# Kernel optimization log

Hardware: AMD Instinct MI355X
Metric: run time of the kernel (lower is better)

The kernel has to match this reference:

```python
import jax, jax.numpy as jnp
import numpy as np

B, L = 2, 256
CHAR, WORD = 8000, 50000
CE, WE, HID, REL = 128, 128, 256, 24
IN_DIM = CE + WE


def _lstm(x, mask, W, U, b):
    # Keras LSTM cell: z = x@W + h@U + b split into (i,f,g,o); masked steps carry state through.
    # x: (B, T, D) float, mask: (B, T) bool
    h0 = jnp.zeros((x.shape[0], U.shape[0]), x.dtype)

    def step(carry, xm):
        h, c = carry
        xt, mt = xm
        z = xt @ W + h @ U + b
        i, f, g, o = jnp.split(z, 4, axis=-1)
        c_new = jax.nn.sigmoid(f) * c + jax.nn.sigmoid(i) * jnp.tanh(g)
        h_new = jax.nn.sigmoid(o) * jnp.tanh(c_new)
        m = mt[:, None]
        h2 = jnp.where(m, h_new, h)
        c2 = jnp.where(m, c_new, c)
        return (h2, c2), h2

    _, hs = jax.lax.scan(step, (h0, h0), (jnp.swapaxes(x, 0, 1), jnp.swapaxes(mask, 0, 1)))
    return jnp.swapaxes(hs, 0, 1)  # (B, T, HID)


def _head(enc, Wu, bu, Wv, bv, Wuv, buv, Wc, bc):
    # Original: tile relu(u) over axis 1 (depends on j) and relu(v) over axis 2 (depends on i),
    # concat -> Dense. Equivalent fused form: split Wuv and broadcast-add the two projections.
    u = jax.nn.relu(enc @ Wu + bu)  # (B, L, E)
    v = jax.nn.relu(enc @ Wv + bv)  # (B, L, E)
    E = Wu.shape[1]
    uv = (jnp.einsum('bjd,de->bje', u, Wuv[:E])[:, None, :, :]
          + jnp.einsum('bid,de->bie', v, Wuv[E:])[:, :, None, :]
          + buv)  # (B, L, L, E)
    return uv @ Wc + bc  # (B, L, L, out)


def setup_inputs() -> dict:
    key = jax.random.key(0)
    ks = jax.random.split(key, 64)

    def w(k, shape):
        return jax.random.normal(k, shape, jnp.float32) * 0.05

    inp = {
        'inputs': jax.random.randint(ks[0], (B, L), 0, CHAR, jnp.int32),
        'input_words': jax.random.randint(ks[1], (B, L), 0, WORD, jnp.int32),
        'input_max_len': L,
        'embed_table': w(ks[2], (CHAR, CE)),
        'word_embed_table': w(ks[3], (WORD, WE)),
        'lstm_fwd_W': w(ks[4], (IN_DIM, 4 * HID)),
        'lstm_fwd_U': w(ks[5], (HID, 4 * HID)),
        'lstm_fwd_b': jnp.zeros((4 * HID,), jnp.float32),
        'lstm_bwd_W': w(ks[6], (IN_DIM, 4 * HID)),
        'lstm_bwd_U': w(ks[7], (HID, 4 * HID)),
        'lstm_bwd_b': jnp.zeros((4 * HID,), jnp.float32),
    }
    i = 8
    for name, out in (('eh', 1), ('hh', REL), ('tt', REL)):
        inp[f'{name}_u_W'] = w(ks[i], (2 * HID, CE)); i += 1
        inp[f'{name}_u_b'] = jnp.zeros((CE,), jnp.float32)
        inp[f'{name}_v_W'] = w(ks[i], (2 * HID, CE)); i += 1
        inp[f'{name}_v_b'] = jnp.zeros((CE,), jnp.float32)
        inp[f'{name}_uv_W'] = w(ks[i], (2 * CE, CE)); i += 1
        inp[f'{name}_uv_b'] = jnp.zeros((CE,), jnp.float32)
        inp[f'{name}_cls_W'] = w(ks[i], (CE, out)); i += 1
        inp[f'{name}_cls_b'] = jnp.zeros((out,), jnp.float32)
    return inp


def reference(inputs, input_words, input_max_len, embed_table, word_embed_table,
              lstm_fwd_W, lstm_fwd_U, lstm_fwd_b, lstm_bwd_W, lstm_bwd_U, lstm_bwd_b,
              eh_u_W, eh_u_b, eh_v_W, eh_v_b, eh_uv_W, eh_uv_b, eh_cls_W, eh_cls_b,
              hh_u_W, hh_u_b, hh_v_W, hh_v_b, hh_uv_W, hh_uv_b, hh_cls_W, hh_cls_b,
              tt_u_W, tt_u_b, tt_v_W, tt_v_b, tt_uv_W, tt_uv_b, tt_cls_W, tt_cls_b):
    mask = inputs != 0  # (B, L)
    x = jnp.concatenate([embed_table[inputs], word_embed_table[input_words]], axis=-1)
    h_fwd = _lstm(x, mask, lstm_fwd_W, lstm_fwd_U, lstm_fwd_b)
    h_bwd = _lstm(x[:, ::-1], mask[:, ::-1], lstm_bwd_W, lstm_bwd_U, lstm_bwd_b)[:, ::-1]
    enc = jnp.concatenate([h_fwd, h_bwd], axis=-1)  # (B, L, 2*HID)
    eh = jax.nn.sigmoid(_head(enc, eh_u_W, eh_u_b, eh_v_W, eh_v_b, eh_uv_W, eh_uv_b, eh_cls_W, eh_cls_b))
    hh = jax.nn.softmax(_head(enc, hh_u_W, hh_u_b, hh_v_W, hh_v_b, hh_uv_W, hh_uv_b, hh_cls_W, hh_cls_b), axis=-1)
    tt = jax.nn.softmax(_head(enc, tt_u_W, tt_u_b, tt_v_W, tt_v_b, tt_uv_W, tt_uv_b, tt_cls_W, tt_cls_b), axis=-1)
    return (eh, hh, tt)
```

## Files before the change

### kernel.cpp

```cpp
#include <hip/hip_runtime.h>
#include <hip/hip_bf16.h>

typedef unsigned short u16;
typedef unsigned int u32;

#define LSEQ 256

constexpr int XW_F  = 0;
constexpr int XW_B  = 524288;
constexpr int HF_O  = 1048576;
constexpr int HB_O  = 1179648;
constexpr int UV_O  = 1310720;
constexpr int PEH_O = 1703936;
constexpr int QEH_O = 1704448;
constexpr int PHH_O = 1704960;
constexpr int QHH_O = 1717248;
constexpr int PTT_O = 1729536;
constexpr int QTT_O = 1741824;
constexpr int TAG_O = 1754112;
constexpr int DT_O  = 1754128;
constexpr int CW_WF = 1754240;
constexpr int CW_UF = 2016384;
constexpr int CW_BF = 2278528;
constexpr int CW_WB = 2279552;
constexpr int CW_UB = 2541696;
constexpr int CW_BB = 2803840;
constexpr int HD0   = 2804864;
constexpr int HDS   = 167424;
constexpr int HD1   = HD0 + HDS;
constexpr int HD2   = HD0 + 2 * HDS;

__device__ __forceinline__ float b2f(u16 u) {
  u32 x = ((u32)u) << 16; float f;
  __builtin_memcpy(&f, &x, 4); return f;
}
__device__ __forceinline__ u16 f2b(float f) {
  u32 x; __builtin_memcpy(&x, &f, 4);
  u32 r = (x + 0x7fffu + ((x >> 16) & 1u)) >> 16;
  return (u16)r;
}
__device__ __forceinline__ float sigm(float x) { return 1.f / (1.f + __expf(-x)); }

__global__ __launch_bounds__(256) void k_detect(const void* __restrict__ etab,
                                                float* __restrict__ ws)
{
  __shared__ int cnt;
  const int tid = threadIdx.x;
  if (tid == 0) cnt = 0;
  __syncthreads();
  const u32 w = ((const u32*)etab)[tid];
  if (w & 0x4000u) atomicAdd(&cnt, 1);
  __syncthreads();
  if (tid == 0) ws[DT_O] = (cnt >= 16) ? 1.0f : 0.0f;
  if (tid < 16) ((u32*)(ws + TAG_O))[tid] = 0u;
}

struct PtrPack { const void* p[30]; };

__global__ __launch_bounds__(256) void k_convert(PtrPack pk, float* __restrict__ ws)
{
  const int cnts[30] = {
    262144, 262144, 1024, 262144, 262144, 1024,
    65536, 128, 65536, 128, 32768, 128, 128, 1,
    65536, 128, 65536, 128, 32768, 128, 3072, 24,
    65536, 128, 65536, 128, 32768, 128, 3072, 24};
  const int dsts[30] = {
    CW_WF, CW_UF, CW_BF, CW_WB, CW_UB, CW_BB,
    HD0, HD0 + 65536, HD0 + 65664, HD0 + 131200, HD0 + 131328, HD0 + 164096, HD0 + 164224, HD0 + 167296,
    HD1, HD1 + 65536, HD1 + 65664, HD1 + 131200, HD1 + 131328, HD1 + 164096, HD1 + 164224, HD1 + 167296,
    HD2, HD2 + 65536, HD2 + 65664, HD2 + 131200, HD2 + 131328, HD2 + 164096, HD2 + 164224, HD2 + 167296};
  const int job = blockIdx.y;
  const int n = cnts[job];
  float* dst = ws + dsts[job];
  const void* src = pk.p[job];
  const bool f32m = ws[DT_O] > 0.5f;
  const int tid = threadIdx.x;
  if (f32m) {
    const float* s = (const float*)src;
    for (int i = blockIdx.x * 256 + tid; i < n; i += 128 * 256) dst[i] = s[i];
  } else {
    const u16* s = (const u16*)src;
    for (int i = blockIdx.x * 256 + tid; i < n; i += 128 * 256) dst[i] = b2f(s[i]);
  }
}

__global__ __launch_bounds__(256) void k_embed_xw(
    const int* __restrict__ toks, const int* __restrict__ wrds,
    const void* __restrict__ etab, const void* __restrict__ wtab,
    float* __restrict__ ws)
{
  __shared__ float xs[2][256];
  const int tid = threadIdx.x, blk = blockIdx.x;
  const bool f32m = ws[DT_O] > 0.5f;
  for (int rr = 0; rr < 2; rr++) {
    const int row = blk * 2 + rr;
    const int id = toks[row], wid = wrds[row];
    float v;
    if (f32m) {
      v = (tid < 128) ? ((const float*)etab)[id * 128 + tid]
                      : ((const float*)wtab)[wid * 128 + (tid - 128)];
    } else {
      v = (tid < 128) ? b2f(((const u16*)etab)[id * 128 + tid])
                      : b2f(((const u16*)wtab)[wid * 128 + (tid - 128)]);
    }
    xs[rr][tid] = v;
  }
  __syncthreads();
  float aF[2][4] = {{0.f,0.f,0.f,0.f},{0.f,0.f,0.f,0.f}};
  float aB[2][4] = {{0.f,0.f,0.f,0.f},{0.f,0.f,0.f,0.f}};
  const float2* Wf2 = (const float2*)(ws + CW_WF);
  const float2* Wb2 = (const float2*)(ws + CW_WB);
  for (int k = 0; k < 256; k++) {
    const float x0 = xs[0][k], x1 = xs[1][k];
    float2 wa = Wf2[k * 512 + tid];
    float2 wb = Wf2[k * 512 + 256 + tid];
    aF[0][0] = fmaf(x0, wa.x, aF[0][0]); aF[0][1] = fmaf(x0, wa.y, aF[0][1]);
    aF[0][2] = fmaf(x0, wb.x, aF[0][2]); aF[0][3] = fmaf(x0, wb.y, aF[0][3]);
    aF[1][0] = fmaf(x1, wa.x, aF[1][0]); aF[1][1] = fmaf(x1, wa.y, aF[1][1]);
    aF[1][2] = fmaf(x1, wb.x, aF[1][2]); aF[1][3] = fmaf(x1, wb.y, aF[1][3]);
    wa = Wb2[k * 512 + tid];
    wb = Wb2[k * 512 + 256 + tid];
    aB[0][0] = fmaf(x0, wa.x, aB[0][0]); aB[0][1] = fmaf(x0, wa.y, aB[0][1]);
    aB[0][2] = fmaf(x0, wb.x, aB[0][2]); aB[0][3] = fmaf(x0, wb.y, aB[0][3]);
    aB[1][0] = fmaf(x1, wa.x, aB[1][0]); aB[1][1] = fmaf(x1, wa.y, aB[1][1]);
    aB[1][2] = fmaf(x1, wb.x, aB[1][2]); aB[1][3] = fmaf(x1, wb.y, aB[1][3]);
  }
  const int c0 = 2 * tid, c2 = 512 + 2 * tid;
  for (int rr = 0; rr < 2; rr++) {
    const int row = blk * 2 + rr;
    float* of = ws + XW_F + row * 1024;
    of[c0]   = aF[rr][0] + ws[CW_BF + c0];
    of[c0+1] = aF[rr][1] + ws[CW_BF + c0 + 1];
    of[c2]   = aF[rr][2] + ws[CW_BF + c2];
    of[c2+1] = aF[rr][3] + ws[CW_BF + c2 + 1];
    float* ob = ws + XW_B + row * 1024;
    ob[c0]   = aB[rr][0] + ws[CW_BB + c0];
    ob[c0+1] = aB[rr][1] + ws[CW_BB + c0 + 1];
    ob[c2]   = aB[rr][2] + ws[CW_BB + c2];
    ob[c2+1] = aB[rr][3] + ws[CW_BB + c2 + 1];
  }
}

__global__ __launch_bounds__(256, 1) void k_lstm(
    const int* __restrict__ toks, float* __restrict__ ws)
{
  __shared__ float2 hsh[256];
  __shared__ float psum[8][256];
  __shared__ float zsh[256];
  const int tid = threadIdx.x;
  const int dir = blockIdx.x >> 3, chunk = blockIdx.x & 7, base = chunk * 32;
  const int q = tid & 31, ksec = tid >> 5, k0 = ksec * 32;
  float* hstep = ws + (dir ? HB_O : HF_O);
  const float* xw = ws + (dir ? XW_B : XW_F);
  const float* Ubase = ws + (dir ? CW_UB : CW_UF);
  u32* tag = (u32*)(ws + TAG_O);

  const int lc0 = 4 * q;
  const int gc0 = ((lc0 >> 5) << 8) + base + (lc0 & 31);
  float4 us[32];
#pragma unroll
  for (int j = 0; j < 32; j++)
    us[j] = *(const float4*)(Ubase + (k0 + j) * 1024 + gc0);

  const int gr = tid >> 5, gj = tid & 31;
  const int rb = tid >> 7, rc = tid & 127;
  const int rgc = ((rc >> 5) << 8) + base + (rc & 31);
  float cReg = 0.f, hReg = 0.f;
  float xwreg = xw[(rb * 256 + (dir ? 255 : 0)) * 1024 + rgc];

  for (int s = 0; s < LSEQ; s++) {
    const int t = dir ? (LSEQ - 1 - s) : s;
    if (s && tid < 8) {
      while ((int)__hip_atomic_load(&tag[dir * 8 + tid], __ATOMIC_ACQUIRE,
                                    __HIP_MEMORY_SCOPE_AGENT) < s)
        __builtin_amdgcn_s_sleep(1);
    }
    __syncthreads();
    if (s) {
      float b0 = __hip_atomic_load(hstep + (s - 1) * 512 + tid,
                                   __ATOMIC_RELAXED, __HIP_MEMORY_SCOPE_AGENT);
      float b1 = __hip_atomic_load(hstep + (s - 1) * 512 + 256 + tid,
                                   __ATOMIC_RELAXED, __HIP_MEMORY_SCOPE_AGENT);
      hsh[tid] = make_float2(b0, b1);
    } else {
      hsh[tid] = make_float2(0.f, 0.f);
    }
    __syncthreads();
    float a00 = 0.f, a01 = 0.f, a02 = 0.f, a03 = 0.f;
    float a10 = 0.f, a11 = 0.f, a12 = 0.f, a13 = 0.f;
#pragma unroll
    for (int j = 0; j < 32; j++) {
      const float2 h = hsh[k0 + j];
      const float4 u = us[j];
      a00 = fmaf(h.x, u.x, a00); a01 = fmaf(h.x, u.y, a01);
      a02 = fmaf(h.x, u.z, a02); a03 = fmaf(h.x, u.w, a03);
      a10 = fmaf(h.y, u.x, a10); a11 = fmaf(h.y, u.y, a11);
      a12 = fmaf(h.y, u.z, a12); a13 = fmaf(h.y, u.w, a13);
    }
    *(float4*)&psum[ksec][lc0]       = make_float4(a00, a01, a02, a03);
    *(float4*)&psum[ksec][128 + lc0] = make_float4(a10, a11, a12, a13);
    __syncthreads();
    {
      float z = xwreg;
#pragma unroll
      for (int ks = 0; ks < 8; ks++) z += psum[ks][rb * 128 + rc];
      zsh[rb * 128 + rc] = z;
    }
    __syncthreads();
    if (tid < 64) {
      const float* zr = &zsh[gr * 128];
      const float zi = zr[gj], zf = zr[32 + gj], zg = zr[64 + gj], zo = zr[96 + gj];
      const float cn = sigm(zf) * cReg + sigm(zi) * tanhf(zg);
      const float hn = sigm(zo) * tanhf(cn);
      if (toks[gr * 256 + t] != 0) { cReg = cn; hReg = hn; }
      __hip_atomic_store(hstep + s * 512 + gr * 256 + base + gj, hReg,
                         __ATOMIC_RELAXED, __HIP_MEMORY_SCOPE_AGENT);
    }
    const int t2 = dir ? (s < 255 ? 254 - s : 0) : (s < 255 ? s + 1 : 255);
    xwreg = xw[(rb * 256 + t2) * 1024 + rgc];
    if (tid == 0)
      __hip_atomic_store(&tag[dir * 8 + chunk], (u32)(s + 1),
                         __ATOMIC_RELEASE, __HIP_MEMORY_SCOPE_AGENT);
  }
}

__global__ __launch_bounds__(256) void k_uv(float* __restrict__ ws)
{
  __shared__ float encs[2][512];
  const int tid = threadIdx.x, blk = blockIdx.x;
  for (int i = tid; i < 1024; i += 256) {
    const int rr = i >> 9, h = i & 511;
    const int row = blk * 2 + rr, b = row >> 8, t = row & 255;
    encs[rr][h] = (h < 256)
        ? ws[HF_O + (t * 2 + b) * 256 + h]
        : ws[HB_O + ((255 - t) * 2 + b) * 256 + (h - 256)];
  }
  __syncthreads();
  const float* wp[3]; float bias[3]; int mats[3], cs[3];
#pragma unroll
  for (int g = 0; g < 3; g++) {
    const int colid = tid + (g << 8);
    mats[g] = colid >> 7; cs[g] = colid & 127;
    const int head = mats[g] >> 1, part = mats[g] & 1;
    wp[g]  = ws + HD0 + head * HDS + (part ? 65664 : 0) + cs[g];
    bias[g] = ws[HD0 + head * HDS + (part ? 131200 : 65536) + cs[g]];
  }
  float acc[3][2] = {{0.f,0.f},{0.f,0.f},{0.f,0.f}};
  for (int k = 0; k < 512; k++) {
    const float e0 = encs[0][k], e1 = encs[1][k];
#pragma unroll
    for (int g = 0; g < 3; g++) {
      const float w = wp[g][k * 128];
      acc[g][0] = fmaf(e0, w, acc[g][0]);
      acc[g][1] = fmaf(e1, w, acc[g][1]);
    }
  }
#pragma unroll
  for (int g = 0; g < 3; g++) {
    for (int rr = 0; rr < 2; rr++) {
      const int row = blk * 2 + rr;
      ws[UV_O + (mats[g] * 512 + row) * 128 + cs[g]] = fmaxf(acc[g][rr] + bias[g], 0.f);
    }
  }
}

__global__ __launch_bounds__(128) void k_pq(float* __restrict__ ws)
{
  __shared__ float us[6][128];
  __shared__ float ash[3][128], qsh[3][128];
  const int row = blockIdx.x, tid = threadIdx.x;
  for (int i = tid; i < 768; i += 128) {
    const int mat = i >> 7, e = i & 127;
    us[mat][e] = ws[UV_O + (mat * 512 + row) * 128 + e];
  }
  __syncthreads();
#pragma unroll
  for (int hd = 0; hd < 3; hd++) {
    const float* W = ws + HD0 + hd * HDS + 131328;
    float a = 0.f, qv = 0.f;
    for (int k = 0; k < 128; k++) {
      a  = fmaf(us[2 * hd][k],     W[k * 128 + tid], a);
      qv = fmaf(us[2 * hd + 1][k], W[(128 + k) * 128 + tid], qv);
    }
    ash[hd][tid] = a + ws[HD0 + hd * HDS + 164096 + tid];
    qsh[hd][tid] = qv;
  }
  __syncthreads();
  if (tid < 98) {
    const float* src; float* dst; const float* Wc; int o, nout;
    if (tid < 2) {
      Wc = ws + HD0 + 164224; nout = 1; o = 0;
      src = (tid == 0) ? ash[0] : qsh[0];
      dst = ws + ((tid == 0) ? PEH_O : QEH_O) + row;
    } else if (tid < 50) {
      Wc = ws + HD1 + 164224; nout = 24;
      if (tid < 26) { o = tid - 2;  src = ash[1]; dst = ws + PHH_O + row * 24 + o; }
      else          { o = tid - 26; src = qsh[1]; dst = ws + QHH_O + row * 24 + o; }
    } else {
      Wc = ws + HD2 + 164224; nout = 24;
      if (tid < 74) { o = tid - 50; src = ash[2]; dst = ws + PTT_O + row * 24 + o; }
      else          { o = tid - 74; src = qsh[2]; dst = ws + QTT_O + row * 24 + o; }
    }
    float acc = 0.f;
    for (int e = 0; e < 128; e++) acc = fmaf(src[e], Wc[e * nout + o], acc);
    *dst = acc;
  }
}

__global__ __launch_bounds__(256) void k_out(const float* __restrict__ ws,
                                             void* __restrict__ outv)
{
  __shared__ float qh[24], qt[24];
  __shared__ float qe_s;
  __shared__ u32 sh[3072], st[3072];
  const bool f32m = ws[DT_O] > 0.5f;
  const int bi = blockIdx.x, b = bi >> 8, i = bi & 255;
  const int j = threadIdx.x;
  if (j < 24)       qh[j] = ws[QHH_O + (b * 256 + i) * 24 + j] + ws[HD1 + 167296 + j];
  else if (j < 48)  qt[j - 24] = ws[QTT_O + (b * 256 + i) * 24 + (j - 24)] + ws[HD2 + 167296 + (j - 24)];
  else if (j == 48) qe_s = ws[QEH_O + b * 256 + i] + ws[HD0 + 167296];
  __syncthreads();
  {
    float v = ws[PEH_O + b * 256 + j] + qe_s;
    v = 1.f / (1.f + __expf(-v));
    if (f32m) ((float*)outv)[(b * 256 + i) * 256 + j] = v;
    else      ((u16*)outv)[(b * 256 + i) * 256 + j] = f2b(v);
  }
  float p[24];
  {
    const float* pp = ws + PHH_O + (b * 256 + j) * 24;
    float mx = -1e30f;
#pragma unroll
    for (int o = 0; o < 24; o++) { p[o] = pp[o] + qh[o]; mx = fmaxf(mx, p[o]); }
    float ssum = 0.f;
#pragma unroll
    for (int o = 0; o < 24; o++) { p[o] = __expf(p[o] - mx); ssum += p[o]; }
    const float inv = 1.f / ssum;
    if (f32m) {
      float* dst = (float*)outv + 131072 + (size_t)(bi * 256 + j) * 24;
#pragma unroll
      for (int m = 0; m < 6; m++)
        ((float4*)dst)[m] = make_float4(p[4*m]*inv, p[4*m+1]*inv, p[4*m+2]*inv, p[4*m+3]*inv);
    } else {
#pragma unroll
      for (int m = 0; m < 12; m++)
        sh[j * 12 + m] = ((u32)f2b(p[2*m+1] * inv) << 16) | (u32)f2b(p[2*m] * inv);
    }
  }
  {
    const float* pp = ws + PTT_O + (b * 256 + j) * 24;
    float mx = -1e30f;
#pragma unroll
    for (int o = 0; o < 24; o++) { p[o] = pp[o] + qt[o]; mx = fmaxf(mx, p[o]); }
    float ssum = 0.f;
#pragma unroll
    for (int o = 0; o < 24; o++) { p[o] = __expf(p[o] - mx); ssum += p[o]; }
    const float inv = 1.f / ssum;
    if (f32m) {
      float* dst = (float*)outv + 3276800 + (size_t)(bi * 256 + j) * 24;
#pragma unroll
      for (int m = 0; m < 6; m++)
        ((float4*)dst)[m] = make_float4(p[4*m]*inv, p[4*m+1]*inv, p[4*m+2]*inv, p[4*m+3]*inv);
    } else {
#pragma unroll
      for (int m = 0; m < 12; m++)
        st[j * 12 + m] = ((u32)f2b(p[2*m+1] * inv) << 16) | (u32)f2b(p[2*m] * inv);
    }
  }
  __syncthreads();
  if (!f32m) {
    u32* outu = (u32*)outv;
    const int baseH = 65536 + bi * 3072;
    const int baseT = 1638400 + bi * 3072;
#pragma unroll
    for (int m = 0; m < 12; m++) {
      outu[baseH + j + 256 * m] = sh[j + 256 * m];
      outu[baseT + j + 256 * m] = st[j + 256 * m];
    }
  }
}

extern "C" void kernel_launch(void* const* d_in, const int* in_sizes, int n_in,
                              void* d_out, int out_size, void* d_ws, size_t ws_size,
                              hipStream_t stream) {
  const int* toks = (const int*)d_in[0];
  const int* wrds = (const int*)d_in[1];
  float* ws = (float*)d_ws;

  k_detect<<<dim3(1), dim3(256), 0, stream>>>(d_in[3], ws);

  PtrPack pk;
  pk.p[0] = d_in[5]; pk.p[1] = d_in[6]; pk.p[2] = d_in[7];
  pk.p[3] = d_in[8]; pk.p[4] = d_in[9]; pk.p[5] = d_in[10];
  for (int h = 0; h < 3; h++)
    for (int a = 0; a < 8; a++)
      pk.p[6 + h * 8 + a] = d_in[11 + h * 8 + a];
  k_convert<<<dim3(128, 30), dim3(256), 0, stream>>>(pk, ws);

  k_embed_xw<<<dim3(256), dim3(256), 0, stream>>>(toks, wrds, d_in[3], d_in[4], ws);
  k_lstm<<<dim3(16), dim3(256), 0, stream>>>(toks, ws);
  k_uv<<<dim3(256), dim3(256), 0, stream>>>(ws);
  k_pq<<<dim3(512), dim3(128), 0, stream>>>(ws);
  k_out<<<dim3(512), dim3(256), 0, stream>>>(ws, d_out);
}
```

Before: 867.7 us.

## Replace LSTM tag-counter handshake with NaN-sentinel polling and enlarge row tiles

```diff
diff --git a/kernel.cpp b/kernel.cpp
--- a/kernel.cpp
+++ b/kernel.cpp
@@ -17,7 +17,6 @@
 constexpr int QHH_O = 1717248;
 constexpr int PTT_O = 1729536;
 constexpr int QTT_O = 1741824;
-constexpr int TAG_O = 1754112;
 constexpr int DT_O  = 1754128;
 constexpr int CW_WF = 1754240;
 constexpr int CW_UF = 2016384;
@@ -39,7 +38,16 @@
   u32 r = (x + 0x7fffu + ((x >> 16) & 1u)) >> 16;
   return (u16)r;
 }
+__device__ __forceinline__ float qnan() {
+  u32 x = 0x7FC00000u; float f; __builtin_memcpy(&f, &x, 4); return f;
+}
 __device__ __forceinline__ float sigm(float x) { return 1.f / (1.f + __expf(-x)); }
+__device__ __forceinline__ float aload(float* p) {
+  return __hip_atomic_load(p, __ATOMIC_RELAXED, __HIP_MEMORY_SCOPE_AGENT);
+}
+__device__ __forceinline__ void astore(float* p, float v) {
+  __hip_atomic_store(p, v, __ATOMIC_RELAXED, __HIP_MEMORY_SCOPE_AGENT);
+}
 
 __global__ __launch_bounds__(256) void k_detect(const void* __restrict__ etab,
                                                 float* __restrict__ ws)
@@ -52,7 +60,6 @@
   if (w & 0x4000u) atomicAdd(&cnt, 1);
   __syncthreads();
   if (tid == 0) ws[DT_O] = (cnt >= 16) ? 1.0f : 0.0f;
-  if (tid < 16) ((u32*)(ws + TAG_O))[tid] = 0u;
 }
 
 struct PtrPack { const void* p[30]; };
@@ -89,11 +96,17 @@
     const void* __restrict__ etab, const void* __restrict__ wtab,
     float* __restrict__ ws)
 {
-  __shared__ float xs[2][256];
+  __shared__ float xs[4][256];
   const int tid = threadIdx.x, blk = blockIdx.x;
+  {
+    float* hz = ws + HF_O + (blk * 256 + tid) * 8;
+    const float nv = qnan();
+#pragma unroll
+    for (int m = 0; m < 8; m++) astore(hz + m, nv);
+  }
   const bool f32m = ws[DT_O] > 0.5f;
-  for (int rr = 0; rr < 2; rr++) {
-    const int row = blk * 2 + rr;
+  for (int rr = 0; rr < 4; rr++) {
+    const int row = blk * 4 + rr;
     const int id = toks[row], wid = wrds[row];
     float v;
     if (f32m) {
@@ -106,28 +119,31 @@
     xs[rr][tid] = v;
   }
   __syncthreads();
-  float aF[2][4] = {{0.f,0.f,0.f,0.f},{0.f,0.f,0.f,0.f}};
-  float aB[2][4] = {{0.f,0.f,0.f,0.f},{0.f,0.f,0.f,0.f}};
+  float aF[4][4], aB[4][4];
+#pragma unroll
+  for (int rr = 0; rr < 4; rr++)
+#pragma unroll
+    for (int c = 0; c < 4; c++) { aF[rr][c] = 0.f; aB[rr][c] = 0.f; }
   const float2* Wf2 = (const float2*)(ws + CW_WF);
   const float2* Wb2 = (const float2*)(ws + CW_WB);
   for (int k = 0; k < 256; k++) {
-    const float x0 = xs[0][k], x1 = xs[1][k];
-    float2 wa = Wf2[k * 512 + tid];
-    float2 wb = Wf2[k * 512 + 256 + tid];
-    aF[0][0] = fmaf(x0, wa.x, aF[0][0]); aF[0][1] = fmaf(x0, wa.y, aF[0][1]);
-    aF[0][2] = fmaf(x0, wb.x, aF[0][2]); aF[0][3] = fmaf(x0, wb.y, aF[0][3]);
-    aF[1][0] = fmaf(x1, wa.x, aF[1][0]); aF[1][1] = fmaf(x1, wa.y, aF[1][1]);
-    aF[1][2] = fmaf(x1, wb.x, aF[1][2]); aF[1][3] = fmaf(x1, wb.y, aF[1][3]);
-    wa = Wb2[k * 512 + tid];
-    wb = Wb2[k * 512 + 256 + tid];
-    aB[0][0] = fmaf(x0, wa.x, aB[0][0]); aB[0][1] = fmaf(x0, wa.y, aB[0][1]);
-    aB[0][2] = fmaf(x0, wb.x, aB[0][2]); aB[0][3] = fmaf(x0, wb.y, aB[0][3]);
-    aB[1][0] = fmaf(x1, wa.x, aB[1][0]); aB[1][1] = fmaf(x1, wa.y, aB[1][1]);
-    aB[1][2] = fmaf(x1, wb.x, aB[1][2]); aB[1][3] = fmaf(x1, wb.y, aB[1][3]);
+    const float2 wfa = Wf2[k * 512 + tid];
+    const float2 wfb = Wf2[k * 512 + 256 + tid];
+    const float2 wba = Wb2[k * 512 + tid];
+    const float2 wbb = Wb2[k * 512 + 256 + tid];
+#pragma unroll
+    for (int rr = 0; rr < 4; rr++) {
+      const float x = xs[rr][k];
+      aF[rr][0] = fmaf(x, wfa.x, aF[rr][0]); aF[rr][1] = fmaf(x, wfa.y, aF[rr][1]);
+      aF[rr][2] = fmaf(x, wfb.x, aF[rr][2]); aF[rr][3] = fmaf(x, wfb.y, aF[rr][3]);
+      aB[rr][0] = fmaf(x, wba.x, aB[rr][0]); aB[rr][1] = fmaf(x, wba.y, aB[rr][1]);
+      aB[rr][2] = fmaf(x, wbb.x, aB[rr][2]); aB[rr][3] = fmaf(x, wbb.y, aB[rr][3]);
+    }
   }
   const int c0 = 2 * tid, c2 = 512 + 2 * tid;
-  for (int rr = 0; rr < 2; rr++) {
-    const int row = blk * 2 + rr;
+#pragma unroll
+  for (int rr = 0; rr < 4; rr++) {
+    const int row = blk * 4 + rr;
     float* of = ws + XW_F + row * 1024;
     of[c0]   = aF[rr][0] + ws[CW_BF + c0];
     of[c0+1] = aF[rr][1] + ws[CW_BF + c0 + 1];
@@ -153,7 +169,6 @@
   float* hstep = ws + (dir ? HB_O : HF_O);
   const float* xw = ws + (dir ? XW_B : XW_F);
   const float* Ubase = ws + (dir ? CW_UB : CW_UF);
-  u32* tag = (u32*)(ws + TAG_O);
 
   const int lc0 = 4 * q;
   const int gc0 = ((lc0 >> 5) << 8) + base + (lc0 & 31);
@@ -170,20 +185,18 @@
 
   for (int s = 0; s < LSEQ; s++) {
     const int t = dir ? (LSEQ - 1 - s) : s;
-    if (s && tid < 8) {
-      while ((int)__hip_atomic_load(&tag[dir * 8 + tid], __ATOMIC_ACQUIRE,
-                                    __HIP_MEMORY_SCOPE_AGENT) < s)
-        __builtin_amdgcn_s_sleep(1);
-    }
-    __syncthreads();
-    if (s) {
-      float b0 = __hip_atomic_load(hstep + (s - 1) * 512 + tid,
-                                   __ATOMIC_RELAXED, __HIP_MEMORY_SCOPE_AGENT);
-      float b1 = __hip_atomic_load(hstep + (s - 1) * 512 + 256 + tid,
-                                   __ATOMIC_RELAXED, __HIP_MEMORY_SCOPE_AGENT);
+    if (s == 0) {
+      hsh[tid] = make_float2(0.f, 0.f);
+    } else {
+      float* p0 = hstep + (s - 1) * 512 + tid;
+      float* p1 = p0 + 256;
+      float b0 = aload(p0);
+      float b1 = aload(p1);
+      while (b0 != b0 || b1 != b1) {
+        if (b0 != b0) b0 = aload(p0);
+        if (b1 != b1) b1 = aload(p1);
+      }
       hsh[tid] = make_float2(b0, b1);
-    } else {
-      hsh[tid] = make_float2(0.f, 0.f);
     }
     __syncthreads();
     float a00 = 0.f, a01 = 0.f, a02 = 0.f, a03 = 0.f;
@@ -213,24 +226,20 @@
       const float cn = sigm(zf) * cReg + sigm(zi) * tanhf(zg);
       const float hn = sigm(zo) * tanhf(cn);
       if (toks[gr * 256 + t] != 0) { cReg = cn; hReg = hn; }
-      __hip_atomic_store(hstep + s * 512 + gr * 256 + base + gj, hReg,
-                         __ATOMIC_RELAXED, __HIP_MEMORY_SCOPE_AGENT);
+      astore(hstep + s * 512 + gr * 256 + base + gj, hReg);
     }
     const int t2 = dir ? (s < 255 ? 254 - s : 0) : (s < 255 ? s + 1 : 255);
     xwreg = xw[(rb * 256 + t2) * 1024 + rgc];
-    if (tid == 0)
-      __hip_atomic_store(&tag[dir * 8 + chunk], (u32)(s + 1),
-                         __ATOMIC_RELEASE, __HIP_MEMORY_SCOPE_AGENT);
   }
 }
 
 __global__ __launch_bounds__(256) void k_uv(float* __restrict__ ws)
 {
-  __shared__ float encs[2][512];
+  __shared__ float encs[4][512];
   const int tid = threadIdx.x, blk = blockIdx.x;
-  for (int i = tid; i < 1024; i += 256) {
+  for (int i = tid; i < 2048; i += 256) {
     const int rr = i >> 9, h = i & 511;
-    const int row = blk * 2 + rr, b = row >> 8, t = row & 255;
+    const int row = blk * 4 + rr, b = row >> 8, t = row & 255;
     encs[rr][h] = (h < 256)
         ? ws[HF_O + (t * 2 + b) * 256 + h]
         : ws[HB_O + ((255 - t) * 2 + b) * 256 + (h - 256)];
@@ -245,65 +254,79 @@
     wp[g]  = ws + HD0 + head * HDS + (part ? 65664 : 0) + cs[g];
     bias[g] = ws[HD0 + head * HDS + (part ? 131200 : 65536) + cs[g]];
   }
-  float acc[3][2] = {{0.f,0.f},{0.f,0.f},{0.f,0.f}};
+  float acc[3][4];
+#pragma unroll
+  for (int g = 0; g < 3; g++)
+#pragma unroll
+    for (int rr = 0; rr < 4; rr++) acc[g][rr] = 0.f;
   for (int k = 0; k < 512; k++) {
-    const float e0 = encs[0][k], e1 = encs[1][k];
+    const float e0 = encs[0][k], e1 = encs[1][k], e2 = encs[2][k], e3 = encs[3][k];
 #pragma unroll
     for (int g = 0; g < 3; g++) {
       const float w = wp[g][k * 128];
       acc[g][0] = fmaf(e0, w, acc[g][0]);
       acc[g][1] = fmaf(e1, w, acc[g][1]);
-    }
-  }
-#pragma unroll
-  for (int g = 0; g < 3; g++) {
+      acc[g][2] = fmaf(e2, w, acc[g][2]);
+      acc[g][3] = fmaf(e3, w, acc[g][3]);
+    }
+  }
+#pragma unroll
+  for (int g = 0; g < 3; g++)
+#pragma unroll
+    for (int rr = 0; rr < 4; rr++) {
+      const int row = blk * 4 + rr;
+      ws[UV_O + (mats[g] * 512 + row) * 128 + cs[g]] = fmaxf(acc[g][rr] + bias[g], 0.f);
+    }
+}
+
+__global__ __launch_bounds__(128) void k_pq(float* __restrict__ ws)
+{
+  __shared__ float us[2][6][128];
+  __shared__ float ash[2][3][128], qsh[2][3][128];
+  const int blk = blockIdx.x, tid = threadIdx.x;
+  for (int i = tid; i < 1536; i += 128) {
+    const int rr = i / 768, rem = i % 768, mat = rem >> 7, e = rem & 127;
+    us[rr][mat][e] = ws[UV_O + (mat * 512 + blk * 2 + rr) * 128 + e];
+  }
+  __syncthreads();
+#pragma unroll
+  for (int hd = 0; hd < 3; hd++) {
+    const float* W = ws + HD0 + hd * HDS + 131328;
+    float a0 = 0.f, a1 = 0.f, q0 = 0.f, q1 = 0.f;
+    for (int k = 0; k < 128; k++) {
+      const float w1 = W[k * 128 + tid];
+      const float w2 = W[(128 + k) * 128 + tid];
+      a0 = fmaf(us[0][2 * hd][k], w1, a0);
+      a1 = fmaf(us[1][2 * hd][k], w1, a1);
+      q0 = fmaf(us[0][2 * hd + 1][k], w2, q0);
+      q1 = fmaf(us[1][2 * hd + 1][k], w2, q1);
+    }
+    const float buv = ws[HD0 + hd * HDS + 164096 + tid];
+    ash[0][hd][tid] = a0 + buv; ash[1][hd][tid] = a1 + buv;
+    qsh[0][hd][tid] = q0;       qsh[1][hd][tid] = q1;
+  }
+  __syncthreads();
+  if (tid < 98) {
     for (int rr = 0; rr < 2; rr++) {
       const int row = blk * 2 + rr;
-      ws[UV_O + (mats[g] * 512 + row) * 128 + cs[g]] = fmaxf(acc[g][rr] + bias[g], 0.f);
-    }
-  }
-}
-
-__global__ __launch_bounds__(128) void k_pq(float* __restrict__ ws)
-{
-  __shared__ float us[6][128];
-  __shared__ float ash[3][128], qsh[3][128];
-  const int row = blockIdx.x, tid = threadIdx.x;
-  for (int i = tid; i < 768; i += 128) {
-    const int mat = i >> 7, e = i & 127;
-    us[mat][e] = ws[UV_O + (mat * 512 + row) * 128 + e];
-  }
-  __syncthreads();
-#pragma unroll
-  for (int hd = 0; hd < 3; hd++) {
-    const float* W = ws + HD0 + hd * HDS + 131328;
-    float a = 0.f, qv = 0.f;
-    for (int k = 0; k < 128; k++) {
-      a  = fmaf(us[2 * hd][k],     W[k * 128 + tid], a);
-      qv = fmaf(us[2 * hd + 1][k], W[(128 + k) * 128 + tid], qv);
-    }
-    ash[hd][tid] = a + ws[HD0 + hd * HDS + 164096 + tid];
-    qsh[hd][tid] = qv;
-  }
-  __syncthreads();
-  if (tid < 98) {
-    const float* src; float* dst; const float* Wc; int o, nout;
-    if (tid < 2) {
-      Wc = ws + HD0 + 164224; nout = 1; o = 0;
-      src = (tid == 0) ? ash[0] : qsh[0];
-      dst = ws + ((tid == 0) ? PEH_O : QEH_O) + row;
-    } else if (tid < 50) {
-      Wc = ws + HD1 + 164224; nout = 24;
-      if (tid < 26) { o = tid - 2;  src = ash[1]; dst = ws + PHH_O + row * 24 + o; }
-      else          { o = tid - 26; src = qsh[1]; dst = ws + QHH_O + row * 24 + o; }
-    } else {
-      Wc = ws + HD2 + 164224; nout = 24;
-      if (tid < 74) { o = tid - 50; src = ash[2]; dst = ws + PTT_O + row * 24 + o; }
-      else          { o = tid - 74; src = qsh[2]; dst = ws + QTT_O + row * 24 + o; }
-    }
-    float acc = 0.f;
-    for (int e = 0; e < 128; e++) acc = fmaf(src[e], Wc[e * nout + o], acc);
-    *dst = acc;
+      const float* src; float* dst; const float* Wc; int o, nout;
+      if (tid < 2) {
+        Wc = ws + HD0 + 164224; nout = 1; o = 0;
+        src = (tid == 0) ? ash[rr][0] : qsh[rr][0];
+        dst = ws + ((tid == 0) ? PEH_O : QEH_O) + row;
+      } else if (tid < 50) {
+        Wc = ws + HD1 + 164224; nout = 24;
+        if (tid < 26) { o = tid - 2;  src = ash[rr][1]; dst = ws + PHH_O + row * 24 + o; }
+        else          { o = tid - 26; src = qsh[rr][1]; dst = ws + QHH_O + row * 24 + o; }
+      } else {
+        Wc = ws + HD2 + 164224; nout = 24;
+        if (tid < 74) { o = tid - 50; src = ash[rr][2]; dst = ws + PTT_O + row * 24 + o; }
+        else          { o = tid - 74; src = qsh[rr][2]; dst = ws + QTT_O + row * 24 + o; }
+      }
+      float acc = 0.f;
+      for (int e = 0; e < 128; e++) acc = fmaf(src[e], Wc[e * nout + o], acc);
+      *dst = acc;
+    }
   }
 }
 
@@ -397,9 +420,9 @@
       pk.p[6 + h * 8 + a] = d_in[11 + h * 8 + a];
   k_convert<<<dim3(128, 30), dim3(256), 0, stream>>>(pk, ws);
 
-  k_embed_xw<<<dim3(256), dim3(256), 0, stream>>>(toks, wrds, d_in[3], d_in[4], ws);
+  k_embed_xw<<<dim3(128), dim3(256), 0, stream>>>(toks, wrds, d_in[3], d_in[4], ws);
   k_lstm<<<dim3(16), dim3(256), 0, stream>>>(toks, ws);
-  k_uv<<<dim3(256), dim3(256), 0, stream>>>(ws);
-  k_pq<<<dim3(512), dim3(128), 0, stream>>>(ws);
+  k_uv<<<dim3(128), dim3(256), 0, stream>>>(ws);
+  k_pq<<<dim3(256), dim3(128), 0, stream>>>(ws);
   k_out<<<dim3(512), dim3(256), 0, stream>>>(ws, d_out);
 }
```

Result: faster. 807.2 us (-7.0%).
